# Kernel optimization log

Hardware: AMD Instinct MI355X
Metric: run time of the kernel (lower is better)

## Reference

```python
import jax, jax.numpy as jnp
import numpy as np

K = 3
PAD = 1

def _conv2d(x, w, b):
    out = jax.lax.conv_general_dilated(x, w, window_strides=(1, 1), padding=((PAD, PAD), (PAD, PAD)), dimension_numbers=('NCHW', 'OIHW', 'NCHW'))
    return out + b[None, :, None, None]

def _deform_conv(x, w_off, b_off, w):
    # DeformConvPack: offsets predicted by a standard 3x3 conv, then bilinear-
    # sampled deformable 3x3 conv (deformable_groups=1, no bias on deform conv).
    B, C, H, W = x.shape
    offset = _conv2d(x, w_off, b_off)              # [B, 2*K*K, H, W]
    off = offset.reshape(B, K * K, 2, H, W)        # mmcv channel order (y, x) per kernel pt
    oy, ox = off[:, :, 0], off[:, :, 1]            # [B, KK, H, W]
    ky, kx = jnp.meshgrid(jnp.arange(K), jnp.arange(K), indexing='ij')
    ky = ky.reshape(K * K, 1, 1).astype(x.dtype)
    kx = kx.reshape(K * K, 1, 1).astype(x.dtype)
    hh = jnp.arange(H, dtype=x.dtype).reshape(1, H, 1)
    ww = jnp.arange(W, dtype=x.dtype).reshape(1, 1, W)
    py = hh + ky - PAD + oy                        # [B, KK, H, W] sample rows
    px = ww + kx - PAD + ox                        # [B, KK, H, W] sample cols

    def sample_one(xb, pyb, pxb):
        # xb: [C, H, W]; bilinear sample with zero padding outside the image.
        xf = xb.reshape(C, H * W)
        y0 = jnp.floor(pyb)
        x0 = jnp.floor(pxb)
        out = jnp.zeros((C, K * K, H, W), xb.dtype)
        for dy in (0.0, 1.0):          # 4 fixed corners
            for dx in (0.0, 1.0):
                yy = y0 + dy
                xx = x0 + dx
                wgt = (1.0 - jnp.abs(pyb - yy)) * (1.0 - jnp.abs(pxb - xx))
                valid = (yy >= 0) & (yy <= H - 1) & (xx >= 0) & (xx <= W - 1)
                yc = jnp.clip(yy, 0, H - 1).astype(jnp.int32)
                xc = jnp.clip(xx, 0, W - 1).astype(jnp.int32)
                idx = (yc * W + xc).reshape(-1)
                g = jnp.take(xf, idx, axis=1).reshape(C, K * K, H, W)
                out = out + g * (wgt * valid.astype(xb.dtype))[None]
        return out                                  # [C, KK, H, W]

    val = jax.vmap(sample_one)(x, py, px)           # [B, C, KK, H, W]
    return jnp.einsum('bckhw,ock->bohw', val, w.reshape(w.shape[0], C, K * K))

def _cam_attn(f):
    # CAM_Calculate (DANet channel attention): CxC softmax over max-stabilized energy.
    B, C, H, W = f.shape
    q = f.reshape(B, C, H * W)
    energy = jnp.einsum('bcn,bdn->bcd', q, q)       # [B, C, C]
    energy_new = jnp.max(energy, axis=-1, keepdims=True) - energy
    return jax.nn.softmax(energy_new, axis=-1)

def _cam_use(f, attn, gamma):
    # CAM_Use: gamma-scaled residual application of a (possibly cross) attention map.
    B, C, H, W = f.shape
    v = f.reshape(B, C, H * W)
    out = jnp.einsum('bcd,bdn->bcn', attn, v).reshape(B, C, H, W)
    return gamma * out + f

def _forward(z0, z1, z2, x0, x1, x2, offw0, offb0, dw0, gamma0, offw1, offb1, dw1, gamma1, offw2, offb2, dw2, gamma2):
    zs = (z0, z1, z2)
    xs = (x0, x1, x2)
    params = ((offw0, offb0, dw0, gamma0), (offw1, offb1, dw1, gamma1), (offw2, offb2, dw2, gamma2))
    z_out, x_out = [], []
    for i in range(3):                              # fixed 3 scales
        zf, xf = zs[i], xs[i]
        w_off, b_off, w, gamma = params[i]
        za = _cam_attn(zf)
        xa = _cam_attn(xf)
        zf = _cam_use(zf, xa, gamma)                # cross attention: z uses x's map
        xf = _cam_use(xf, za, gamma)
        z_out.append(_deform_conv(zf, w_off, b_off, w))
        x_out.append(_deform_conv(xf, w_off, b_off, w))
    return jnp.stack(z_out), jnp.stack(x_out)       # [3,B,256,15,15], [3,B,256,31,31]

def setup_inputs():
    key = jax.random.key(0)
    B, C, HZ, HX = 32, 256, 15, 31
    ks = jax.random.split(key, 12)
    inp = {}
    for i in range(3):
        inp[f'z{i}'] = jax.random.normal(ks[i], (B, C, HZ, HZ), jnp.float32)
        inp[f'x{i}'] = jax.random.normal(ks[3 + i], (B, C, HX, HX), jnp.float32)
        inp[f'offw{i}'] = jax.random.normal(ks[6 + i], (2 * 9, C, 3, 3), jnp.float32) * 0.01
        inp[f'offb{i}'] = jnp.zeros((2 * 9,), jnp.float32)
        inp[f'dw{i}'] = jax.random.normal(ks[9 + i], (C, C, 3, 3), jnp.float32) * (1.0 / np.sqrt(C * 9))
        inp[f'gamma{i}'] = jnp.full((1,), 0.5, jnp.float32)
    return inp

def reference(z0, z1, z2, x0, x1, x2, offw0, offb0, dw0, gamma0, offw1, offb1, dw1, gamma1, offw2, offb2, dw2, gamma2):
    return _forward(z0, z1, z2, x0, x1, x2, offw0, offb0, dw0, gamma0, offw1, offb1, dw1, gamma1, offw2, offb2, dw2, gamma2)
```

## Files before the change

kernel.cpp:

```cpp
#include <hip/hip_runtime.h>
#include <math.h>


#define BB 32

typedef _Float16 f16x8 __attribute__((ext_vector_type(8)));
typedef _Float16 f16x4 __attribute__((ext_vector_type(4)));
typedef float    f32x4 __attribute__((ext_vector_type(4)));

__global__ void prep_kernel(const float* __restrict__ dw,
                            const float* __restrict__ offw,
                            _Float16* __restrict__ WTs,
                            float* __restrict__ offwP) {
    int bx = blockIdx.x;
    int t  = threadIdx.x;
    if (bx < 2304) {
        int idx = bx * 256 + t;
        int j    = idx & 7;
        int lane = (idx >> 3) & 63;
        int ot   = (idx >> 9) & 15;
        int ks   = idx >> 13;
        int o  = ot * 16 + (lane & 15);
        int kk = ks * 32 + (lane >> 4) * 8 + j;
        int c   = kk & 255;
        int kyx = kk >> 8;
        WTs[idx] = (_Float16)dw[(size_t)o * 2304 + c * 9 + kyx];
    } else {
        int r = bx - 2304;
        int kyx = r / 18, j = r % 18;
        offwP[((size_t)(kyx * 18 + j)) * 256 + t] = offw[((size_t)(j * 256 + t)) * 9 + kyx];
    }
}

__global__ void energy_kernel(const float* __restrict__ f,
                              float* __restrict__ energy, int N) {
    int b  = blockIdx.z;
    int c0 = blockIdx.x * 64;
    int d0 = blockIdx.y * 64;
    int t  = threadIdx.x;
    __shared__ __align__(16) float A[32][68];
    __shared__ __align__(16) float Bs[32][68];
    float acc[4][4] = {};
    int cc0 = (t & 15) * 4;
    int dd0 = (t >> 4) * 4;
    const float* fb = f + (size_t)b * 256 * N;
    for (int n0 = 0; n0 < N; n0 += 32) {
        #pragma unroll
        for (int pass = 0; pass < 8; ++pass) {
            int idx = pass * 256 + t;
            int nn = idx & 31;
            int rr = idx >> 5;
            int n = n0 + nn;
            float va = (n < N) ? fb[(size_t)(c0 + rr) * N + n] : 0.f;
            float vb = (n < N) ? fb[(size_t)(d0 + rr) * N + n] : 0.f;
            A[nn][rr]  = va;
            Bs[nn][rr] = vb;
        }
        __syncthreads();
        #pragma unroll 8
        for (int nn = 0; nn < 32; ++nn) {
            float4 a4 = *(const float4*)&A[nn][cc0];
            float4 b4 = *(const float4*)&Bs[nn][dd0];
            float av[4] = {a4.x, a4.y, a4.z, a4.w};
            float bv[4] = {b4.x, b4.y, b4.z, b4.w};
            #pragma unroll
            for (int i = 0; i < 4; ++i)
                #pragma unroll
                for (int j = 0; j < 4; ++j)
                    acc[i][j] += av[i] * bv[j];
        }
        __syncthreads();
    }
    #pragma unroll
    for (int i = 0; i < 4; ++i) {
        float4 o4 = {acc[i][0], acc[i][1], acc[i][2], acc[i][3]};
        *(float4*)&energy[((size_t)b * 256 + (c0 + cc0 + i)) * 256 + d0 + dd0] = o4;
    }
}

__global__ void softmax_kernel(float* __restrict__ attn) {
    int row = blockIdx.x;
    int t = threadIdx.x;
    float e = attn[(size_t)row * 256 + t];
    __shared__ float red[256];
    red[t] = e;
    __syncthreads();
    for (int s = 128; s > 0; s >>= 1) {
        if (t < s) red[t] = fminf(red[t], red[t + s]);
        __syncthreads();
    }
    float mn = red[0];
    __syncthreads();
    float p = __expf(mn - e);
    red[t] = p;
    __syncthreads();
    for (int s = 128; s > 0; s >>= 1) {
        if (t < s) red[t] += red[t + s];
        __syncthreads();
    }
    float inv = 1.f / red[0];
    attn[(size_t)row * 256 + t] = p * inv;
}

__global__ void cam_use_kernel(const float* __restrict__ f,
                               const float* __restrict__ attn,
                               const float* __restrict__ gamma,
                               float* __restrict__ g, int N) {
    int b  = blockIdx.z;
    int n0 = blockIdx.x * 64;
    int c0 = blockIdx.y * 64;
    int t  = threadIdx.x;
    __shared__ __align__(16) float At[32][68];
    __shared__ __align__(16) float Ft[32][68];
    float acc[4][4] = {};
    int cc0 = (t & 15) * 4;
    int nn0 = (t >> 4) * 4;
    const float* fb = f + (size_t)b * 256 * N;
    const float* ab = attn + (size_t)b * 256 * 256;
    for (int d0 = 0; d0 < 256; d0 += 32) {
        #pragma unroll
        for (int pass = 0; pass < 8; ++pass) {
            int idx = pass * 256 + t;
            int dd = idx & 31;
            int cc = idx >> 5;
            At[dd][cc] = ab[(size_t)(c0 + cc) * 256 + d0 + dd];
        }
        #pragma unroll
        for (int pass = 0; pass < 8; ++pass) {
            int idx = pass * 256 + t;
            int nn = idx & 63;
            int dd = idx >> 6;
            int n = n0 + nn;
            Ft[dd][nn] = (n < N) ? fb[(size_t)(d0 + dd) * N + n] : 0.f;
        }
        __syncthreads();
        #pragma unroll 8
        for (int dd = 0; dd < 32; ++dd) {
            float4 a4 = *(const float4*)&At[dd][cc0];
            float4 f4 = *(const float4*)&Ft[dd][nn0];
            float av[4] = {a4.x, a4.y, a4.z, a4.w};
            float fv[4] = {f4.x, f4.y, f4.z, f4.w};
            #pragma unroll
            for (int i = 0; i < 4; ++i)
                #pragma unroll
                for (int j = 0; j < 4; ++j)
                    acc[i][j] += av[i] * fv[j];
        }
        __syncthreads();
    }
    float gam = gamma[0];
    #pragma unroll
    for (int j = 0; j < 4; ++j) {
        int n = n0 + nn0 + j;
        if (n >= N) continue;
        float4 o4;
        o4.x = fb[(size_t)(c0 + cc0 + 0) * N + n] + gam * acc[0][j];
        o4.y = fb[(size_t)(c0 + cc0 + 1) * N + n] + gam * acc[1][j];
        o4.z = fb[(size_t)(c0 + cc0 + 2) * N + n] + gam * acc[2][j];
        o4.w = fb[(size_t)(c0 + cc0 + 3) * N + n] + gam * acc[3][j];
        *(float4*)&g[((size_t)b * N + n) * 256 + c0 + cc0] = o4;
    }
}

__global__ void offset_kernel(const float* __restrict__ gx_,
                              const float* __restrict__ gz_,
                              const float* __restrict__ offwP,
                              const float* __restrict__ offb,
                              float* __restrict__ pyxx_,
                              float* __restrict__ pyxz_) {
    const int bx = blockIdx.x;
    const float* g; float* pyxg; int H, W, p0;
    if (bx < 16) { g = gx_; pyxg = pyxx_; H = 31; W = 31; p0 = bx * 64; }
    else         { g = gz_; pyxg = pyxz_; H = 15; W = 15; p0 = (bx - 16) * 64; }
    const int N = H * W;
    const int b  = blockIdx.y;
    const int t  = threadIdx.x;
    const int pixl = t & 63;
    const int q = __builtin_amdgcn_readfirstlane(t >> 6);
    const int pix = p0 + pixl;
    float acc[18];
    #pragma unroll
    for (int j = 0; j < 18; ++j) acc[j] = 0.f;
    const float* gb = g + (size_t)b * N * 256;
    if (pix < N) {
        int h = pix / W, w_ = pix % W;
        for (int kyx = 0; kyx < 9; ++kyx) {
            int y = h + kyx / 3 - 1;
            int x = w_ + kyx % 3 - 1;
            if (y < 0 || y >= H || x < 0 || x >= W) continue;
            const float* grow = gb + (size_t)(y * W + x) * 256 + q * 64;
            const float* wrow = offwP + (size_t)kyx * 18 * 256 + q * 64;
            for (int c4 = 0; c4 < 16; ++c4) {
                float4 g4 = *(const float4*)(grow + c4 * 4);
                #pragma unroll
                for (int j = 0; j < 18; ++j) {
                    float4 w4 = *(const float4*)(wrow + (size_t)j * 256 + c4 * 4);
                    acc[j] += g4.x * w4.x + g4.y * w4.y + g4.z * w4.z + g4.w * w4.w;
                }
            }
        }
    }
    __shared__ float red[4][64][18];
    #pragma unroll
    for (int j = 0; j < 18; ++j) red[q][pixl][j] = acc[j];
    __syncthreads();
    for (int idx = t; idx < 64 * 18; idx += 256) {
        int pl = idx / 18, j = idx % 18;
        int pp = p0 + pl;
        if (pp >= N) continue;
        float s = red[0][pl][j] + red[1][pl][j] + red[2][pl][j] + red[3][pl][j] + offb[j];
        int k = j >> 1, comp = j & 1;
        int h = pp / W, w_ = pp % W;
        float base = comp ? (float)(w_ + (k % 3) - 1) : (float)(h + (k / 3) - 1);
        pyxg[((size_t)b * N + pp) * 18 + j] = base + s;
    }
}

__global__ __launch_bounds__(256, 2)
void deform_mfma_kernel(const float* __restrict__ gx_,
                        const float* __restrict__ gz_,
                        const _Float16* __restrict__ WTs,
                        const float* __restrict__ pyxx_,
                        const float* __restrict__ pyxz_,
                        float* __restrict__ outx_,
                        float* __restrict__ outz_) {
    const int bx = blockIdx.x;
    const int b  = blockIdx.y;
    const float* g; const float* pyxg; float* out; int H, W, p0;
    if (bx < 16) { g = gx_; pyxg = pyxx_; out = outx_; H = 31; W = 31; p0 = bx * 64; }
    else         { g = gz_; pyxg = pyxz_; out = outz_; H = 15; W = 15; p0 = (bx - 16) * 64; }
    const int N = H * W;
    const int t    = threadIdx.x;
    const int lane = t & 63;
    const int wv   = t >> 6;

    __shared__ __align__(16) _Float16 valq[2][32 * 64 * 8];
    __shared__ __align__(16) float4  metaW[576];
    __shared__ __align__(8)  ushort4 metaR[576];

    const float* gb = g + (size_t)b * N * 256;
    const float Hm1 = (float)(H - 1), Wm1 = (float)(W - 1);

    for (int idx = t; idx < 576; idx += 256) {
        int pixl = idx / 9, kyx = idx - pixl * 9;
        int pix = p0 + pixl;
        float py = -1.0e6f, px = -1.0e6f;
        if (pix < N) {
            const float* pp = pyxg + ((size_t)b * N + pix) * 18 + kyx * 2;
            py = pp[0]; px = pp[1];
        }
        float y0f = floorf(py), x0f = floorf(px);
        float fy = py - y0f, fx = px - x0f;
        bool vy0 = (y0f >= 0.f) && (y0f <= Hm1);
        bool vy1 = (y0f + 1.f >= 0.f) && (y0f + 1.f <= Hm1);
        bool vx0 = (x0f >= 0.f) && (x0f <= Wm1);
        bool vx1 = (x0f + 1.f >= 0.f) && (x0f + 1.f <= Wm1);
        int iy0 = min(max((int)y0f, 0), H - 1);
        int iy1 = min(max((int)y0f + 1, 0), H - 1);
        int ix0 = min(max((int)x0f, 0), W - 1);
        int ix1 = min(max((int)x0f + 1, 0), W - 1);
        float w00 = (vy0 && vx0) ? (1.f - fy) * (1.f - fx) : 0.f;
        float w01 = (vy0 && vx1) ? (1.f - fy) * fx : 0.f;
        float w10 = (vy1 && vx0) ? fy * (1.f - fx) : 0.f;
        float w11 = (vy1 && vx1) ? fy * fx : 0.f;
        metaW[idx] = make_float4(w00, w01, w10, w11);
        metaR[idx] = make_ushort4((unsigned short)(iy0 * W + ix0),
                                  (unsigned short)(iy0 * W + ix1),
                                  (unsigned short)(iy1 * W + ix0),
                                  (unsigned short)(iy1 * W + ix1));
    }

    f32x4 acc[4][4];
    #pragma unroll
    for (int i = 0; i < 4; ++i)
        #pragma unroll
        for (int j = 0; j < 4; ++j)
            acc[i][j] = (f32x4){0.f, 0.f, 0.f, 0.f};

    auto SAMPLE = [&](int kyx, int bufsel) {
        _Float16* vq = &valq[bufsel][0];
        #pragma unroll
        for (int s = 0; s < 2; ++s) {
            int item = t + s * 256;
            int pixl = item >> 3;
            int f4   = item & 7;
            float4  w4 = metaW[pixl * 9 + kyx];
            ushort4 r4 = metaR[pixl * 9 + kyx];
            const float* p00 = gb + (size_t)r4.x * 256 + f4 * 4;
            const float* p01 = gb + (size_t)r4.y * 256 + f4 * 4;
            const float* p10 = gb + (size_t)r4.z * 256 + f4 * 4;
            const float* p11 = gb + (size_t)r4.w * 256 + f4 * 4;
            const int halfoff = (f4 & 1) * 4;
            const int kk8base = f4 >> 1;
            #pragma unroll
            for (int gq = 0; gq < 8; ++gq) {
                float4 a  = *(const float4*)(p00 + gq * 32);
                float4 bq = *(const float4*)(p01 + gq * 32);
                float4 cq = *(const float4*)(p10 + gq * 32);
                float4 dq = *(const float4*)(p11 + gq * 32);
                f16x4 h;
                h[0] = (_Float16)(w4.x * a.x + w4.y * bq.x + w4.z * cq.x + w4.w * dq.x);
                h[1] = (_Float16)(w4.x * a.y + w4.y * bq.y + w4.z * cq.y + w4.w * dq.y);
                h[2] = (_Float16)(w4.x * a.z + w4.y * bq.z + w4.z * cq.z + w4.w * dq.z);
                h[3] = (_Float16)(w4.x * a.w + w4.y * bq.w + w4.z * cq.w + w4.w * dq.w);
                int kk8 = kk8base + gq * 4;
                *(f16x4*)&vq[(kk8 * 64 + pixl) * 8 + halfoff] = h;
            }
        }
    };

    auto MFMA9 = [&](int kyx, int bufsel) {
        const _Float16* vq = &valq[bufsel][0];
        #pragma unroll 4
        for (int cs = 0; cs < 8; ++cs) {
            int ks = kyx * 8 + cs;
            f16x8 afrag[4], bfrag[4];
            #pragma unroll
            for (int ot = 0; ot < 4; ++ot)
                afrag[ot] = *(const f16x8*)(WTs +
                    (((size_t)ks * 16 + wv * 4 + ot) * 64 + lane) * 8);
            #pragma unroll
            for (int pt = 0; pt < 4; ++pt)
                bfrag[pt] = *(const f16x8*)(vq +
                    (((cs * 4 + (lane >> 4)) * 64) + pt * 16 + (lane & 15)) * 8);
            #pragma unroll
            for (int ot = 0; ot < 4; ++ot)
                #pragma unroll
                for (int pt = 0; pt < 4; ++pt)
                    acc[ot][pt] = __builtin_amdgcn_mfma_f32_16x16x32_f16(
                        afrag[ot], bfrag[pt], acc[ot][pt], 0, 0, 0);
        }
    };

    __syncthreads();
    SAMPLE(0, 0);
    for (int kyx = 0; kyx < 9; ++kyx) {
        __syncthreads();
        if (kyx < 8) SAMPLE(kyx + 1, (kyx + 1) & 1);
        MFMA9(kyx, kyx & 1);
    }

    __syncthreads();
    float* tp = (float*)&valq[0][0] + wv * 4096;
    const int pcol = lane & 15;
    const int quad = lane >> 4;
    #pragma unroll
    for (int ot = 0; ot < 4; ++ot)
        #pragma unroll
        for (int pt = 0; pt < 4; ++pt)
            #pragma unroll
            for (int r = 0; r < 4; ++r)
                tp[(ot * 16 + quad * 4 + r) * 64 + pt * 16 + pcol] = acc[ot][pt][r];
    float* ob = out + (size_t)b * 256 * N;
    #pragma unroll
    for (int i = 0; i < 16; ++i) {
        int o   = wv * 64 + i * 4 + quad;
        int px0 = p0 + pcol * 4;
        float4 v = *(const float4*)&tp[(i * 4 + quad) * 64 + pcol * 4];
        if (px0 + 3 < N) {
            *(float4*)&ob[(size_t)o * N + px0] = v;
        } else if (px0 < N) {
            float vv[4] = {v.x, v.y, v.z, v.w};
            #pragma unroll
            for (int j = 0; j < 4; ++j)
                if (px0 + j < N) ob[(size_t)o * N + px0 + j] = vv[j];
        }
    }
}

extern "C" void kernel_launch(void* const* d_in, const int* in_sizes, int n_in,
                              void* d_out, int out_size, void* d_ws, size_t ws_size,
                              hipStream_t stream) {
    const int Nz = 225, Nx = 961;
    const size_t ZSZ = (size_t)BB * 256 * Nz;
    const size_t XSZ = (size_t)BB * 256 * Nx;

    bool dict_order = (in_sizes[1] == (int)XSZ);
    const float *z[3], *x[3], *offw[3], *offb[3], *dw[3], *gamma[3];
    for (int i = 0; i < 3; ++i) {
        if (dict_order) {
            z[i]     = (const float*)d_in[i * 6 + 0];
            x[i]     = (const float*)d_in[i * 6 + 1];
            offw[i]  = (const float*)d_in[i * 6 + 2];
            offb[i]  = (const float*)d_in[i * 6 + 3];
            dw[i]    = (const float*)d_in[i * 6 + 4];
            gamma[i] = (const float*)d_in[i * 6 + 5];
        } else {
            z[i]     = (const float*)d_in[i];
            x[i]     = (const float*)d_in[3 + i];
            offw[i]  = (const float*)d_in[6 + i * 4 + 0];
            offb[i]  = (const float*)d_in[6 + i * 4 + 1];
            dw[i]    = (const float*)d_in[6 + i * 4 + 2];
            gamma[i] = (const float*)d_in[6 + i * 4 + 3];
        }
    }

    float* ws = (float*)d_ws;
    _Float16* WTs3 = (_Float16*)ws;
    float* offwP3 = ws + 884736;
    float* attn_z = offwP3 + 3 * 41472;
    float* attn_x = attn_z + 2097152;
    float* gz     = attn_x + 2097152;
    float* gx     = gz + 1843200;
    float* pyz    = gx + 7872512;
    float* pyxx   = pyz + 129600;

    for (int i = 0; i < 3; ++i)
        prep_kernel<<<2466, 256, 0, stream>>>(dw[i], offw[i],
                                              WTs3 + (size_t)i * 589824,
                                              offwP3 + (size_t)i * 41472);

    float* out_f = (float*)d_out;
    for (int i = 0; i < 3; ++i) {
        energy_kernel<<<dim3(4, 4, BB), 256, 0, stream>>>(z[i], attn_z, Nz);
        energy_kernel<<<dim3(4, 4, BB), 256, 0, stream>>>(x[i], attn_x, Nx);
        softmax_kernel<<<BB * 256, 256, 0, stream>>>(attn_z);
        softmax_kernel<<<BB * 256, 256, 0, stream>>>(attn_x);
        cam_use_kernel<<<dim3(4, 4, BB), 256, 0, stream>>>(z[i], attn_x, gamma[i], gz, Nz);
        cam_use_kernel<<<dim3(16, 4, BB), 256, 0, stream>>>(x[i], attn_z, gamma[i], gx, Nx);

        offset_kernel<<<dim3(20, BB), 256, 0, stream>>>(
            gx, gz, offwP3 + (size_t)i * 41472, offb[i], pyxx, pyz);

        float* oz = out_f + (size_t)i * ZSZ;
        float* ox = out_f + 3 * ZSZ + (size_t)i * XSZ;
        deform_mfma_kernel<<<dim3(20, BB), 256, 0, stream>>>(
            gx, gz, WTs3 + (size_t)i * 589824, pyxx, pyz, ox, oz);
    }
}
```

Baseline: 2.052 ms.

## Compute CAM energy Gram matrix with split-fp16 MFMA instead of fp32 FMA

Replaces the scalar fp32 outer-product energy kernel with one using 16x16x32 fp16 MFMA instructions. Each fp32 input is split into high and low fp16 parts, and three MFMAs (hi*hi, hi*lo, lo*hi) recover near-fp32 accuracy. Global loads are vectorised to float4 with a scalar fallback at the tail. The aim is to cut the ALU cost of the channel-attention energy matrices. The trade-offs are slightly lower precision feeding the softmax, and float4 loads from rows whose start need not be 16-byte aligned.

```diff
diff --git a/kernel.cpp b/kernel.cpp
--- a/kernel.cpp
+++ b/kernel.cpp
@@ -32,50 +32,88 @@
     }
 }
 
-__global__ void energy_kernel(const float* __restrict__ f,
-                              float* __restrict__ energy, int N) {
-    int b  = blockIdx.z;
-    int c0 = blockIdx.x * 64;
-    int d0 = blockIdx.y * 64;
-    int t  = threadIdx.x;
-    __shared__ __align__(16) float A[32][68];
-    __shared__ __align__(16) float Bs[32][68];
-    float acc[4][4] = {};
-    int cc0 = (t & 15) * 4;
-    int dd0 = (t >> 4) * 4;
+#define ERS 40
+__global__ __launch_bounds__(256, 4)
+void energy_mfma_kernel(const float* __restrict__ f,
+                        float* __restrict__ energy, int N) {
+    const int b  = blockIdx.z;
+    const int c0 = blockIdx.x * 64;
+    const int d0 = blockIdx.y * 64;
+    const int t  = threadIdx.x;
+    const int lane = t & 63;
+    const int wv   = t >> 6;
+
+    __shared__ __align__(16) _Float16 Ah[64][ERS];
+    __shared__ __align__(16) _Float16 Al[64][ERS];
+    __shared__ __align__(16) _Float16 Bh[64][ERS];
+    __shared__ __align__(16) _Float16 Bl[64][ERS];
+
     const float* fb = f + (size_t)b * 256 * N;
+
+    f32x4 acc[4];
+    #pragma unroll
+    for (int j = 0; j < 4; ++j) acc[j] = (f32x4){0.f, 0.f, 0.f, 0.f};
+
+    const int ra     = t >> 2;
+    const int c4base = t & 3;
+
     for (int n0 = 0; n0 < N; n0 += 32) {
-        #pragma unroll
-        for (int pass = 0; pass < 8; ++pass) {
-            int idx = pass * 256 + t;
-            int nn = idx & 31;
-            int rr = idx >> 5;
-            int n = n0 + nn;
-            float va = (n < N) ? fb[(size_t)(c0 + rr) * N + n] : 0.f;
-            float vb = (n < N) ? fb[(size_t)(d0 + rr) * N + n] : 0.f;
-            A[nn][rr]  = va;
-            Bs[nn][rr] = vb;
-        }
-        __syncthreads();
-        #pragma unroll 8
-        for (int nn = 0; nn < 32; ++nn) {
-            float4 a4 = *(const float4*)&A[nn][cc0];
-            float4 b4 = *(const float4*)&Bs[nn][dd0];
-            float av[4] = {a4.x, a4.y, a4.z, a4.w};
-            float bv[4] = {b4.x, b4.y, b4.z, b4.w};
-            #pragma unroll
-            for (int i = 0; i < 4; ++i)
+        __syncthreads();
+        #pragma unroll
+        for (int s = 0; s < 2; ++s) {
+            int c4 = c4base + 4 * s;
+            int n  = n0 + c4 * 4;
+            const float* rowc = fb + (size_t)(c0 + ra) * N;
+            const float* rowd = fb + (size_t)(d0 + ra) * N;
+            float va[4], vb[4];
+            if (n + 3 < N) {
+                float4 t4 = *(const float4*)(rowc + n);
+                va[0] = t4.x; va[1] = t4.y; va[2] = t4.z; va[3] = t4.w;
+                float4 u4 = *(const float4*)(rowd + n);
+                vb[0] = u4.x; vb[1] = u4.y; vb[2] = u4.z; vb[3] = u4.w;
+            } else {
                 #pragma unroll
-                for (int j = 0; j < 4; ++j)
-                    acc[i][j] += av[i] * bv[j];
-        }
-        __syncthreads();
-    }
-    #pragma unroll
-    for (int i = 0; i < 4; ++i) {
-        float4 o4 = {acc[i][0], acc[i][1], acc[i][2], acc[i][3]};
-        *(float4*)&energy[((size_t)b * 256 + (c0 + cc0 + i)) * 256 + d0 + dd0] = o4;
-    }
+                for (int k = 0; k < 4; ++k) {
+                    va[k] = (n + k < N) ? rowc[n + k] : 0.f;
+                    vb[k] = (n + k < N) ? rowd[n + k] : 0.f;
+                }
+            }
+            f16x4 ha, la, hb, lb;
+            #pragma unroll
+            for (int k = 0; k < 4; ++k) {
+                ha[k] = (_Float16)va[k];
+                la[k] = (_Float16)(va[k] - (float)ha[k]);
+                hb[k] = (_Float16)vb[k];
+                lb[k] = (_Float16)(vb[k] - (float)hb[k]);
+            }
+            *(f16x4*)&Ah[ra][c4 * 4] = ha;
+            *(f16x4*)&Al[ra][c4 * 4] = la;
+            *(f16x4*)&Bh[ra][c4 * 4] = hb;
+            *(f16x4*)&Bl[ra][c4 * 4] = lb;
+        }
+        __syncthreads();
+        const int fr = lane & 15;
+        const int fq = lane >> 4;
+        f16x8 a_h = *(const f16x8*)&Ah[wv * 16 + fr][fq * 8];
+        f16x8 a_l = *(const f16x8*)&Al[wv * 16 + fr][fq * 8];
+        #pragma unroll
+        for (int pt = 0; pt < 4; ++pt) {
+            f16x8 b_h = *(const f16x8*)&Bh[pt * 16 + fr][fq * 8];
+            f16x8 b_l = *(const f16x8*)&Bl[pt * 16 + fr][fq * 8];
+            acc[pt] = __builtin_amdgcn_mfma_f32_16x16x32_f16(a_h, b_h, acc[pt], 0, 0, 0);
+            acc[pt] = __builtin_amdgcn_mfma_f32_16x16x32_f16(a_h, b_l, acc[pt], 0, 0, 0);
+            acc[pt] = __builtin_amdgcn_mfma_f32_16x16x32_f16(a_l, b_h, acc[pt], 0, 0, 0);
+        }
+    }
+
+    const int fr = lane & 15;
+    const int fq = lane >> 4;
+    #pragma unroll
+    for (int pt = 0; pt < 4; ++pt)
+        #pragma unroll
+        for (int r = 0; r < 4; ++r)
+            energy[((size_t)b * 256 + (c0 + wv * 16 + fq * 4 + r)) * 256
+                   + d0 + pt * 16 + fr] = acc[pt][r];
 }
 
 __global__ void softmax_kernel(float* __restrict__ attn) {
@@ -412,8 +450,8 @@
 
     float* out_f = (float*)d_out;
     for (int i = 0; i < 3; ++i) {
-        energy_kernel<<<dim3(4, 4, BB), 256, 0, stream>>>(z[i], attn_z, Nz);
-        energy_kernel<<<dim3(4, 4, BB), 256, 0, stream>>>(x[i], attn_x, Nx);
+        energy_mfma_kernel<<<dim3(4, 4, BB), 256, 0, stream>>>(z[i], attn_z, Nz);
+        energy_mfma_kernel<<<dim3(4, 4, BB), 256, 0, stream>>>(x[i], attn_x, Nx);
         softmax_kernel<<<BB * 256, 256, 0, stream>>>(attn_z);
         softmax_kernel<<<BB * 256, 256, 0, stream>>>(attn_x);
         cam_use_kernel<<<dim3(4, 4, BB), 256, 0, stream>>>(z[i], attn_x, gamma[i], gz, Nz);
```

New measurement: 1.696 ms. -17.3%, faster.
